# Kernel tuning notes

Hardware: AMD Instinct MI355X
Metric: run time of the kernel (lower is better)

## Reference

```python
import jax, jax.numpy as jnp
import numpy as np


def _step(state):
    # state: [B, H, W] in {0.0, 1.0}
    p = jnp.pad(state, ((0, 0), (1, 1), (1, 1)))
    neighbors = (p[:, :-2, :-2] + p[:, :-2, 1:-1] + p[:, :-2, 2:]
                 + p[:, 1:-1, :-2] + p[:, 1:-1, 2:]
                 + p[:, 2:, :-2] + p[:, 2:, 1:-1] + p[:, 2:, 2:])
    alive = state > 0.5
    survives = alive & ((neighbors == 2.0) | (neighbors == 3.0))
    born = (~alive) & (neighbors == 3.0)
    return jnp.where(survives | born, jnp.ones_like(state), jnp.zeros_like(state))


def setup_inputs() -> dict:
    key = jax.random.key(0)
    k1, k2 = jax.random.split(key)
    B, H, W = 32, 1024, 1024
    # Binary occupancy grids in {0.0, 1.0} as the rule expects
    initial_state = (jax.random.uniform(k1, (B, H, W)) > 0.5).astype(jnp.float32)
    target = (jax.random.uniform(k2, (B, H, W)) > 0.5).astype(jnp.float32)
    return {"initial_state": initial_state, "target": target, "generations": 8}


def reference(initial_state, target, generations):
    state = initial_state
    for _ in range(generations):  # small fixed unroll, strict sequential dependency
        state = _step(state)
    error = state - target
    loss = jnp.mean(error * error)
    live_cells = state.sum()
    max_abs_error = jnp.abs(error).max()
    return loss, state, target, live_cells, max_abs_error
```

## Files before the change

kernel.cpp:

```cpp
#include <hip/hip_runtime.h>
#include <cstdint>

typedef unsigned long long u64;

#define BATCH   32
#define H       1024
#define W       1024
#define WPR     16
#define TR      64
#define HALO    8
#define BR      (TR + 2*HALO)
#define BRP     (BR + 2)
#define WP      (WPR + 2)
#define THREADS 512
#define NWAVES  (THREADS/64)
#define GENS    8
#define GRID    (BATCH * (H / TR))
#define NTOT    33554432ULL

__device__ __forceinline__ u64 shflxor64(u64 v, int m) {
    return (u64)__shfl_xor((long long)v, m, 64);
}

__global__ __launch_bounds__(THREADS)
void gol_fused(const float* __restrict__ in_state,
               const float* __restrict__ target,
               float* __restrict__ out,
               u64* __restrict__ counters)
{
    __shared__ u64 buf[2][BRP][WP];
    __shared__ unsigned int wsum[NWAVES];

    const int tile = blockIdx.x;
    const int tpb  = H / TR;
    const int b    = tile / tpb;
    const int r0   = (tile - b * tpb) * TR;

    const int tid  = threadIdx.x;
    const int wave = tid >> 6;
    const int lane = tid & 63;

    for (int i = tid; i < 2 * BRP * WP; i += THREADS)
        ((u64*)buf)[i] = 0ULL;
    __syncthreads();

    const size_t boff = (size_t)b * H * W;
    const float* inb  = in_state + boff;

    const int sub   = lane & 15;
    const int wsub  = lane >> 4;
    for (int br = wave; br < BR; br += NWAVES) {
        int gr = r0 - HALO + br;
        if (gr < 0 || gr >= H) continue;
        const float4* rowp4 = (const float4*)(inb + (size_t)gr * W);
        #pragma unroll
        for (int g = 0; g < 4; ++g) {
            float4 f = rowp4[g * 64 + lane];
            u64 nib = (u64)((f.x > 0.5f) | ((f.y > 0.5f) << 1) |
                            ((f.z > 0.5f) << 2) | ((f.w > 0.5f) << 3));
            u64 v = nib << (sub * 4);
            v |= shflxor64(v, 1);
            v |= shflxor64(v, 2);
            v |= shflxor64(v, 4);
            v |= shflxor64(v, 8);
            if (sub == 0)
                buf[0][br + 1][g * 4 + wsub + 1] = v;
        }
    }
    __syncthreads();

    int cur = 0;
    for (int step = 0; step < GENS; ++step) {
        for (int idx = tid; idx < BR * WPR; idx += THREADS) {
            int br = idx >> 4;
            int c  = (idx & 15) + 1;
            int r  = br + 1;
            int gr = r0 - HALO + br;

            u64 uL = buf[cur][r-1][c-1], uC = buf[cur][r-1][c], uR = buf[cur][r-1][c+1];
            u64 mL = buf[cur][r  ][c-1], mC = buf[cur][r  ][c], mR = buf[cur][r  ][c+1];
            u64 dL = buf[cur][r+1][c-1], dC = buf[cur][r+1][c], dR = buf[cur][r+1][c+1];

            u64 uw = (uC << 1) | (uL >> 63), ue = (uC >> 1) | (uR << 63);
            u64 mw = (mC << 1) | (mL >> 63), me = (mC >> 1) | (mR << 63);
            u64 dw = (dC << 1) | (dL >> 63), de = (dC >> 1) | (dR << 63);
            u64 o0 = uw ^ uC ^ ue, t0 = (uw & uC) | (ue & (uw ^ uC));
            u64 o1 = mw ^ mC ^ me, t1 = (mw & mC) | (me & (mw ^ mC));
            u64 o2 = dw ^ dC ^ de, t2 = (dw & dC) | (de & (dw ^ dC));

            u64 oa = o0 ^ o1 ^ o2;
            u64 oc = (o0 & o1) | (o2 & (o0 ^ o1));
            u64 ts = t0 ^ t1 ^ t2;
            u64 tc = (t0 & t1) | (t2 & (t0 ^ t1));
            u64 b1 = oc ^ ts;
            u64 cc = oc & ts;
            u64 b2 = cc ^ tc;
            u64 b3 = cc & tc;
            u64 eq3 = oa & b1 & ~(b2 | b3);
            u64 eq4 = (~oa) & (~b1) & b2 & (~b3);
            u64 nxtw = eq3 | (mC & eq4);

            buf[cur ^ 1][r][c] = (gr >= 0 && gr < H) ? nxtw : 0ULL;
        }
        __syncthreads();
        cur ^= 1;
    }

    float* o_state = out + 1;
    float* o_tgt   = out + 1 + NTOT;

    unsigned int mism = 0, live = 0;
    for (int lr = wave; lr < TR; lr += NWAVES) {
        int br = HALO + lr;
        int gr = r0 + lr;
        size_t rowbase = boff + (size_t)gr * W;
        const u64* wrow = &buf[cur][br + 1][1];
        const float* trow = target + rowbase;
        float* osrow = o_state + rowbase;
        float* otrow = o_tgt + rowbase;
        #pragma unroll
        for (int g = 0; g < 4; ++g) {
            int k = g * 64 + lane;
            if (k < 255) {
                int bitbase = 4 * k + 3;
                int w0 = bitbase >> 6;
                int sh = bitbase & 63;
                u64 lo = wrow[w0];
                u64 hi = wrow[w0 + 1];
                unsigned bits = (unsigned)(((lo >> sh) | (hi << (64 - sh))) & 0xFULL);
                float4 t = *(const float4*)(trow + bitbase);
                unsigned tb = (unsigned)((t.x > 0.5f) | ((t.y > 0.5f) << 1) |
                                         ((t.z > 0.5f) << 2) | ((t.w > 0.5f) << 3));
                mism += (unsigned)__popc(bits ^ tb);
                live += (unsigned)__popc(bits);
                float4 sv;
                sv.x = (float)(bits & 1u);
                sv.y = (float)((bits >> 1) & 1u);
                sv.z = (float)((bits >> 2) & 1u);
                sv.w = (float)((bits >> 3) & 1u);
                *(float4*)(osrow + bitbase) = sv;
                *(float4*)(otrow + bitbase) = t;
            } else {
                u64 wfirst = wrow[0];
                u64 wlast  = wrow[15];
                unsigned hb  = (unsigned)(wfirst & 7ULL);
                unsigned tbit = (unsigned)(wlast >> 63);
                float t0 = trow[0], t1 = trow[1], t2 = trow[2], t3 = trow[1023];
                unsigned htb = (unsigned)((t0 > 0.5f) | ((t1 > 0.5f) << 1) | ((t2 > 0.5f) << 2));
                unsigned ttb = (unsigned)(t3 > 0.5f);
                mism += (unsigned)__popc(hb ^ htb) + (tbit ^ ttb);
                live += (unsigned)__popc(hb) + tbit;
                osrow[0] = (float)(hb & 1u);
                osrow[1] = (float)((hb >> 1) & 1u);
                osrow[2] = (float)((hb >> 2) & 1u);
                osrow[1023] = (float)tbit;
                otrow[0] = t0; otrow[1] = t1; otrow[2] = t2; otrow[1023] = t3;
            }
        }
    }

    unsigned int comb = (mism << 16) | live;
    #pragma unroll
    for (int m = 1; m < 64; m <<= 1)
        comb += (unsigned int)__shfl_xor((int)comb, m, 64);
    if (lane == 0) wsum[wave] = comb;
    __syncthreads();

    if (tid == 0) {
        unsigned int bm = 0, bl = 0;
        #pragma unroll
        for (int i = 0; i < NWAVES; ++i) {
            bm += wsum[i] >> 16;
            bl += wsum[i] & 0xFFFFu;
        }
        atomicAdd(counters, ((u64)bm << 32) | (u64)bl);
    }
}

__global__ void gol_finalize(const u64* __restrict__ counters,
                             float* __restrict__ out)
{
    u64 c = *counters;
    unsigned int mism = (unsigned int)(c >> 32);
    unsigned int live = (unsigned int)(c & 0xFFFFFFFFULL);
    out[0]            = (float)((double)mism / (double)NTOT);
    out[1 + 2*NTOT]   = (float)live;
    out[2 + 2*NTOT]   = (mism > 0) ? 1.0f : 0.0f;
}

extern "C" void kernel_launch(void* const* d_in, const int* in_sizes, int n_in,
                              void* d_out, int out_size, void* d_ws, size_t ws_size,
                              hipStream_t stream) {
    (void)in_sizes; (void)n_in; (void)out_size; (void)ws_size;
    const float* in_state = (const float*)d_in[0];
    const float* target   = (const float*)d_in[1];
    float* out = (float*)d_out;
    u64* counters = (u64*)d_ws;

    hipMemsetAsync(d_ws, 0, sizeof(u64), stream);

    gol_fused<<<dim3(GRID), dim3(THREADS), 0, stream>>>(in_state, target, out, counters);
    gol_finalize<<<1, 1, 0, stream>>>(counters, out);
}
```

Measured before the change: 462.9 us.

## Split bit-packing into a separate pre-pass kernel and halve life tile height

Adds a separate kernel that packs the float input grid into 64-bit bitmasks in workspace once, so the life kernel loads the compact packed rows instead of re-reading and re-packing halo float rows from global memory. The life tile shrinks to 32 rows with 256 threads, and its loops are fully unrolled. This removes the redundant float reads of the halo rows, but adds a kernel launch and a packed intermediate round trip. Halo recomputation overhead grows relative to tile size (16 halo rows per 32 output rows).

```diff
diff --git a/kernel.cpp b/kernel.cpp
--- a/kernel.cpp
+++ b/kernel.cpp
@@ -7,52 +7,33 @@
 #define H       1024
 #define W       1024
 #define WPR     16
-#define TR      64
+#define GENS    8
 #define HALO    8
-#define BR      (TR + 2*HALO)
-#define BRP     (BR + 2)
-#define WP      (WPR + 2)
-#define THREADS 512
-#define NWAVES  (THREADS/64)
-#define GENS    8
-#define GRID    (BATCH * (H / TR))
 #define NTOT    33554432ULL
+
+#define PK_THREADS 256
+#define PK_WAVES   4
+#define PK_ROWS_PER_BLOCK 32
+#define PK_GRID    ((BATCH * H) / PK_ROWS_PER_BLOCK)
 
 __device__ __forceinline__ u64 shflxor64(u64 v, int m) {
     return (u64)__shfl_xor((long long)v, m, 64);
 }
 
-__global__ __launch_bounds__(THREADS)
-void gol_fused(const float* __restrict__ in_state,
-               const float* __restrict__ target,
-               float* __restrict__ out,
-               u64* __restrict__ counters)
+__global__ __launch_bounds__(PK_THREADS)
+void gol_pack(const float* __restrict__ in_state, u64* __restrict__ packed)
 {
-    __shared__ u64 buf[2][BRP][WP];
-    __shared__ unsigned int wsum[NWAVES];
-
-    const int tile = blockIdx.x;
-    const int tpb  = H / TR;
-    const int b    = tile / tpb;
-    const int r0   = (tile - b * tpb) * TR;
-
     const int tid  = threadIdx.x;
     const int wave = tid >> 6;
     const int lane = tid & 63;
-
-    for (int i = tid; i < 2 * BRP * WP; i += THREADS)
-        ((u64*)buf)[i] = 0ULL;
-    __syncthreads();
-
-    const size_t boff = (size_t)b * H * W;
-    const float* inb  = in_state + boff;
-
-    const int sub   = lane & 15;
-    const int wsub  = lane >> 4;
-    for (int br = wave; br < BR; br += NWAVES) {
-        int gr = r0 - HALO + br;
-        if (gr < 0 || gr >= H) continue;
-        const float4* rowp4 = (const float4*)(inb + (size_t)gr * W);
+    const int sub  = lane & 15;
+    const int wsub = lane >> 4;
+
+    const int row0 = blockIdx.x * PK_ROWS_PER_BLOCK;
+    for (int rr = wave; rr < PK_ROWS_PER_BLOCK; rr += PK_WAVES) {
+        int row = row0 + rr;
+        const float4* rowp4 = (const float4*)(in_state + (size_t)row * W);
+        u64* prow = packed + (size_t)row * WPR;
         #pragma unroll
         for (int g = 0; g < 4; ++g) {
             float4 f = rowp4[g * 64 + lane];
@@ -64,14 +45,58 @@
             v |= shflxor64(v, 4);
             v |= shflxor64(v, 8);
             if (sub == 0)
-                buf[0][br + 1][g * 4 + wsub + 1] = v;
-        }
+                prow[g * 4 + wsub] = v;
+        }
+    }
+}
+
+#define TR      32
+#define BR      (TR + 2*HALO)
+#define BRP     (BR + 2)
+#define WP      (WPR + 2)
+#define THREADS 256
+#define NWAVES  (THREADS/64)
+#define GRID    (BATCH * (H / TR))
+
+__global__ __launch_bounds__(THREADS)
+void gol_life(const u64* __restrict__ packed,
+              const float* __restrict__ target,
+              float* __restrict__ out,
+              u64* __restrict__ counters)
+{
+    __shared__ u64 buf[2][BRP][WP];
+    __shared__ unsigned int wsum[NWAVES];
+
+    const int tile = blockIdx.x;
+    const int tpb  = H / TR;
+    const int b    = tile / tpb;
+    const int r0   = (tile - b * tpb) * TR;
+
+    const int tid  = threadIdx.x;
+    const int wave = tid >> 6;
+    const int lane = tid & 63;
+
+    for (int i = tid; i < 2 * BRP * WP; i += THREADS)
+        ((u64*)buf)[i] = 0ULL;
+    __syncthreads();
+
+    const u64* packedb = packed + (size_t)b * H * WPR;
+    #pragma unroll
+    for (int k = 0; k < (BR * WPR) / THREADS; ++k) {
+        int idx = tid + k * THREADS;
+        int br = idx >> 4;
+        int c  = idx & 15;
+        int gr = r0 - HALO + br;
+        if (gr >= 0 && gr < H)
+            buf[0][br + 1][c + 1] = packedb[(size_t)gr * WPR + c];
     }
     __syncthreads();
 
     int cur = 0;
     for (int step = 0; step < GENS; ++step) {
-        for (int idx = tid; idx < BR * WPR; idx += THREADS) {
+        #pragma unroll
+        for (int k = 0; k < (BR * WPR) / THREADS; ++k) {
+            int idx = tid + k * THREADS;
             int br = idx >> 4;
             int c  = (idx & 15) + 1;
             int r  = br + 1;
@@ -108,6 +133,7 @@
 
     float* o_state = out + 1;
     float* o_tgt   = out + 1 + NTOT;
+    const size_t boff = (size_t)b * H * W;
 
     unsigned int mism = 0, live = 0;
     for (int lr = wave; lr < TR; lr += NWAVES) {
@@ -143,7 +169,7 @@
             } else {
                 u64 wfirst = wrow[0];
                 u64 wlast  = wrow[15];
-                unsigned hb  = (unsigned)(wfirst & 7ULL);
+                unsigned hb   = (unsigned)(wfirst & 7ULL);
                 unsigned tbit = (unsigned)(wlast >> 63);
                 float t0 = trow[0], t1 = trow[1], t2 = trow[2], t3 = trow[1023];
                 unsigned htb = (unsigned)((t0 > 0.5f) | ((t1 > 0.5f) << 1) | ((t2 > 0.5f) << 2));
@@ -195,10 +221,13 @@
     const float* in_state = (const float*)d_in[0];
     const float* target   = (const float*)d_in[1];
     float* out = (float*)d_out;
+
     u64* counters = (u64*)d_ws;
+    u64* packed   = (u64*)((char*)d_ws + 256);
 
     hipMemsetAsync(d_ws, 0, sizeof(u64), stream);
 
-    gol_fused<<<dim3(GRID), dim3(THREADS), 0, stream>>>(in_state, target, out, counters);
+    gol_pack<<<dim3(PK_GRID), dim3(PK_THREADS), 0, stream>>>(in_state, packed);
+    gol_life<<<dim3(GRID), dim3(THREADS), 0, stream>>>(packed, target, out, counters);
     gol_finalize<<<1, 1, 0, stream>>>(counters, out);
 }
```

Result: no change. 468.5 us (+1.2%).
